# Optimization experiments

Measured on AMD Instinct MI355X. Metric: run time of the kernel, lower is better.

The kernel has to match this reference:

```python
import jax, jax.numpy as jnp
import numpy as np

D_MODEL = 4096
NUM_EXPERTS = 64
TOP_K = 2


def setup_inputs() -> dict:
    key = jax.random.key(0)
    kx, kw, kb = jax.random.split(key, 3)
    x = jax.random.normal(kx, (4, 4096, D_MODEL), dtype=jnp.float32)
    # nn.Linear(d_model, num_experts): weight [E, D], bias [E]
    bound = 1.0 / np.sqrt(D_MODEL)
    W = jax.random.uniform(kw, (NUM_EXPERTS, D_MODEL), dtype=jnp.float32, minval=-bound, maxval=bound)
    b = jax.random.uniform(kb, (NUM_EXPERTS,), dtype=jnp.float32, minval=-bound, maxval=bound)
    return {"x": x, "W": W, "b": b}


def reference(x, W, b):
    # logits = gate(x): [B, S, E]
    logits = jnp.einsum("bsd,ed->bse", x, W) + b
    scores = jax.nn.softmax(logits, axis=-1)
    topk_scores, topk_idx = jax.lax.top_k(scores, TOP_K)  # [B,S,K]
    # scatter top-k scores back into a dense [B,S,E] dispatch mask
    onehot = jax.nn.one_hot(topk_idx, NUM_EXPERTS, dtype=scores.dtype)  # [B,S,K,E]
    dispatch_mask = jnp.einsum("bske,bsk->bse", onehot, topk_scores)
    return dispatch_mask
```

## Files before the change

kernel.cpp:

```cpp
#include <hip/hip_runtime.h>
#include <hip/hip_bf16.h>
#include <math.h>
#include <stdint.h>

#define DM 4096
#define NEXP 64
#define BK 32
#define NCH (DM / BK)
#define TOKW 64
#define NSLICE 8
#define CHPS (NCH / NSLICE)
#define NTOK 16384

typedef short bf16x8 __attribute__((ext_vector_type(8)));
typedef float f32x4  __attribute__((ext_vector_type(4)));

__device__ __forceinline__ void split2(float f0, float f1, uint32_t& hw, uint32_t& lw) {
    float2 ff; ff.x = f0; ff.y = f1;
    __hip_bfloat162 h = __float22bfloat162_rn(ff);
    union { __hip_bfloat162 b; uint32_t u; } ch; ch.b = h;
    hw = ch.u;
    float h0 = __bfloat162float(h.x);
    float h1 = __bfloat162float(h.y);
    float2 gg; gg.x = f0 - h0; gg.y = f1 - h1;
    __hip_bfloat162 l = __float22bfloat162_rn(gg);
    union { __hip_bfloat162 b; uint32_t u; } cl; cl.b = l;
    lw = cl.u;
}

__global__ __launch_bounds__(256) void wsplit_kernel(const float* __restrict__ W,
                                                     char* __restrict__ blob) {
    const int c   = blockIdx.x;
    const int tid = threadIdx.x;
    const int e   = tid >> 2;
    const int g   = tid & 3;

    const float* src = W + (size_t)e * DM + c * BK + g * 8;
    float x[8];
    *(float4*)(x)     = *(const float4*)(src);
    *(float4*)(x + 4) = *(const float4*)(src + 4);

    uint32_t hiw[4], low[4];
#pragma unroll
    for (int j = 0; j < 4; ++j) split2(x[2 * j], x[2 * j + 1], hiw[j], low[j]);

    const int ln = (e & 15) | (g << 4);
    const int n4 = e >> 4;
    const size_t base = (size_t)c * 8192 + (size_t)n4 * 1024 + (size_t)ln * 16;
    *(uint4*)(blob + base)        = *(uint4*)hiw;
    *(uint4*)(blob + base + 4096) = *(uint4*)low;
}

__global__ __launch_bounds__(1024) void router_mfma_kernel(
    const float* __restrict__ X,
    const char* __restrict__ blob,
    const float* __restrict__ Bv,
    float* __restrict__ out)
{
    __shared__ float part[NSLICE][TOKW][NEXP];

    const int tid  = threadIdx.x;
    const int lane = tid & 63;
    const int wv   = tid >> 6;
    const int eh   = wv & 1;
    const int ksl  = wv >> 1;
    const long tok0 = (long)blockIdx.x * TOKW;

    const int tk = lane & 15;
    const int kg = lane >> 4;

    const float* a0 = X + (size_t)(tok0 + tk) * DM + kg * 8;

    f32x4 acc[4][2];
#pragma unroll
    for (int m = 0; m < 4; ++m)
#pragma unroll
        for (int n = 0; n < 2; ++n) acc[m][n] = (f32x4)0.0f;

    const int c0 = ksl * CHPS;
#pragma unroll 1
    for (int ci = 0; ci < CHPS; ++ci) {
        const int c = c0 + ci;

        float ar[4][8];
#pragma unroll
        for (int m = 0; m < 4; ++m) {
            const float* p = a0 + (size_t)m * (16 * DM) + c * BK;
            *(float4*)(ar[m])     = *(const float4*)(p);
            *(float4*)(ar[m] + 4) = *(const float4*)(p + 4);
        }

        bf16x8 ah[4], al[4];
#pragma unroll
        for (int m = 0; m < 4; ++m) {
            uint32_t hw[4], lw[4];
#pragma unroll
            for (int j = 0; j < 4; ++j)
                split2(ar[m][2 * j], ar[m][2 * j + 1], hw[j], lw[j]);
            ah[m] = *(bf16x8*)hw;
            al[m] = *(bf16x8*)lw;
        }

        const char* bb = blob + (size_t)c * 8192;
#pragma unroll
        for (int n = 0; n < 2; ++n) {
            const size_t bo = (size_t)(eh * 2 + n) * 1024 + (size_t)lane * 16;
            bf16x8 bh = *(const bf16x8*)(bb + bo);
            bf16x8 bl = *(const bf16x8*)(bb + 4096 + bo);
#pragma unroll
            for (int m = 0; m < 4; ++m) {
                acc[m][n] = __builtin_amdgcn_mfma_f32_16x16x32_bf16(ah[m], bh, acc[m][n], 0, 0, 0);
                acc[m][n] = __builtin_amdgcn_mfma_f32_16x16x32_bf16(ah[m], bl, acc[m][n], 0, 0, 0);
                acc[m][n] = __builtin_amdgcn_mfma_f32_16x16x32_bf16(al[m], bh, acc[m][n], 0, 0, 0);
            }
        }
    }

#pragma unroll
    for (int m = 0; m < 4; ++m)
#pragma unroll
        for (int n = 0; n < 2; ++n)
#pragma unroll
            for (int r = 0; r < 4; ++r)
                part[ksl][m * 16 + kg * 4 + r][eh * 32 + n * 16 + tk] = acc[m][n][r];
    __syncthreads();

#pragma unroll
    for (int i = 0; i < 4; ++i) {
        const int cell = tid + i * 1024;
        const int t = cell >> 6;
        const int e = cell & 63;
        float s = part[0][t][e];
#pragma unroll
        for (int w = 1; w < NSLICE; ++w) s += part[w][t][e];
        part[0][t][e] = s;
    }
    __syncthreads();

    const float bias = Bv[lane];
#pragma unroll 1
    for (int j = 0; j < 4; ++j) {
        const int t = wv * 4 + j;
        float v = part[0][t][lane] + bias;

        float m1 = v;        int i1 = lane;
        float m2 = -3.4e38f; int i2 = 127;
#pragma unroll
        for (int s = 1; s < 64; s <<= 1) {
            float om1 = __shfl_xor(m1, s, 64);
            int   oi1 = __shfl_xor(i1, s, 64);
            float om2 = __shfl_xor(m2, s, 64);
            int   oi2 = __shfl_xor(i2, s, 64);
            bool bw2 = (om1 > m1) || (om1 == m1 && oi1 < i1);
            float l1v = bw2 ? m1 : om1;  int l1i = bw2 ? i1 : oi1;
            float w2v = bw2 ? om2 : m2;  int w2i = bw2 ? oi2 : i2;
            if (bw2) { m1 = om1; i1 = oi1; }
            bool tw = (l1v > w2v) || (l1v == w2v && l1i < w2i);
            m2 = tw ? l1v : w2v;  i2 = tw ? l1i : w2i;
        }

        float p = expf(v - m1);
        float ssum = p;
#pragma unroll
        for (int s = 1; s < 64; s <<= 1) ssum += __shfl_xor(ssum, s, 64);

        float sc = (lane == i1 || lane == i2) ? (p / ssum) : 0.0f;
        out[(size_t)(tok0 + t) * NEXP + lane] = sc;
    }
}

extern "C" void kernel_launch(void* const* d_in, const int* in_sizes, int n_in,
                              void* d_out, int out_size, void* d_ws, size_t ws_size,
                              hipStream_t stream) {
    const float* X  = (const float*)d_in[0];
    const float* W  = (const float*)d_in[1];
    const float* Bv = (const float*)d_in[2];
    float* out = (float*)d_out;

    char* blob = (char*)d_ws;
    wsplit_kernel<<<dim3(NCH), dim3(256), 0, stream>>>(W, blob);

    router_mfma_kernel<<<dim3(NTOK / TOKW), dim3(1024), 0, stream>>>(X, blob, Bv, out);
}
```

Before: 85.05 us.

## Stream X tiles into LDS with async double-buffered loads and retile waves

Activation tiles are now staged into LDS using global_load_lds with a two-deep ring buffer and explicit vmcnt waits. This overlaps the global load of the next K-chunks with the fp32-to-bf16 split and the MFMA work. The block shrinks to 32 tokens and 8 waves, each wave covering all 64 experts over one K-slice, which doubles the grid and targets 4 blocks per CU. The cost is hand-tuned waitcnt counts that depend on the compiler's instruction order, more re-reads of the weight blob across blocks, and 64KB of LDS per block, which may limit occupancy.

```diff
diff --git a/kernel.cpp b/kernel.cpp
--- a/kernel.cpp
+++ b/kernel.cpp
@@ -7,13 +7,16 @@
 #define NEXP 64
 #define BK 32
 #define NCH (DM / BK)
-#define TOKW 64
-#define NSLICE 8
-#define CHPS (NCH / NSLICE)
+#define TOKW 32
+#define KSPLIT 8
+#define CHPS (NCH / KSPLIT)
 #define NTOK 16384
 
 typedef short bf16x8 __attribute__((ext_vector_type(8)));
 typedef float f32x4  __attribute__((ext_vector_type(4)));
+
+#define WAITVM12() { asm volatile("s_waitcnt vmcnt(12)" ::: "memory"); __builtin_amdgcn_sched_barrier(0); }
+#define WAITVM8()  { asm volatile("s_waitcnt vmcnt(8)"  ::: "memory"); __builtin_amdgcn_sched_barrier(0); }
 
 __device__ __forceinline__ void split2(float f0, float f1, uint32_t& hw, uint32_t& lw) {
     float2 ff; ff.x = f0; ff.y = f1;
@@ -51,97 +54,118 @@
     *(uint4*)(blob + base + 4096) = *(uint4*)low;
 }
 
-__global__ __launch_bounds__(1024) void router_mfma_kernel(
+__global__ __launch_bounds__(512, 4) void router_mfma_kernel(
     const float* __restrict__ X,
     const char* __restrict__ blob,
     const float* __restrict__ Bv,
     float* __restrict__ out)
 {
-    __shared__ float part[NSLICE][TOKW][NEXP];
+    __shared__ __align__(16) char smem[65536];
 
     const int tid  = threadIdx.x;
     const int lane = tid & 63;
     const int wv   = tid >> 6;
-    const int eh   = wv & 1;
-    const int ksl  = wv >> 1;
     const long tok0 = (long)blockIdx.x * TOKW;
 
     const int tk = lane & 15;
     const int kg = lane >> 4;
 
-    const float* a0 = X + (size_t)(tok0 + tk) * DM + kg * 8;
-
-    f32x4 acc[4][2];
-#pragma unroll
-    for (int m = 0; m < 4; ++m)
-#pragma unroll
-        for (int n = 0; n < 2; ++n) acc[m][n] = (f32x4)0.0f;
-
-    const int c0 = ksl * CHPS;
+    char* wbase = smem + wv * 8192;
+    const int c0 = wv * CHPS;
+
+    auto stage = [&](int c, int b) {
+#pragma unroll
+        for (int m = 0; m < 2; ++m)
+#pragma unroll
+            for (int h = 0; h < 2; ++h) {
+                const float* src = X + (size_t)(tok0 + m * 16 + tk) * DM + c * BK + kg * 8 + h * 4;
+                char* dst = wbase + b * 4096 + (m * 2 + h) * 1024 + lane * 16;
+                __builtin_amdgcn_global_load_lds(
+                    (const __attribute__((address_space(1))) void*)src,
+                    (__attribute__((address_space(3))) void*)dst, 16, 0, 0);
+            }
+    };
+
+    f32x4 acc[2][4];
+#pragma unroll
+    for (int m = 0; m < 2; ++m)
+#pragma unroll
+        for (int n = 0; n < 4; ++n) acc[m][n] = (f32x4)0.0f;
+
+    stage(c0 + 0, 0);
+    stage(c0 + 1, 1);
+
 #pragma unroll 1
     for (int ci = 0; ci < CHPS; ++ci) {
         const int c = c0 + ci;
-
-        float ar[4][8];
-#pragma unroll
-        for (int m = 0; m < 4; ++m) {
-            const float* p = a0 + (size_t)m * (16 * DM) + c * BK;
-            *(float4*)(ar[m])     = *(const float4*)(p);
-            *(float4*)(ar[m] + 4) = *(const float4*)(p + 4);
+        const int b = ci & 1;
+
+        const char* bb = blob + (size_t)c * 8192;
+        bf16x8 bh[4], bl[4];
+#pragma unroll
+        for (int n = 0; n < 4; ++n) {
+            const size_t bo = (size_t)n * 1024 + (size_t)lane * 16;
+            bh[n] = *(const bf16x8*)(bb + bo);
+            bl[n] = *(const bf16x8*)(bb + 4096 + bo);
         }
 
-        bf16x8 ah[4], al[4];
-#pragma unroll
-        for (int m = 0; m < 4; ++m) {
+        if (ci < CHPS - 1) { WAITVM12(); } else { WAITVM8(); }
+
+        bf16x8 ah[2], al[2];
+#pragma unroll
+        for (int m = 0; m < 2; ++m) {
+            const char* fb = wbase + b * 4096 + m * 2048 + lane * 16;
+            f32x4 f0 = *(const f32x4*)(fb);
+            f32x4 f1 = *(const f32x4*)(fb + 1024);
             uint32_t hw[4], lw[4];
-#pragma unroll
-            for (int j = 0; j < 4; ++j)
-                split2(ar[m][2 * j], ar[m][2 * j + 1], hw[j], lw[j]);
+            split2(f0.x, f0.y, hw[0], lw[0]);
+            split2(f0.z, f0.w, hw[1], lw[1]);
+            split2(f1.x, f1.y, hw[2], lw[2]);
+            split2(f1.z, f1.w, hw[3], lw[3]);
             ah[m] = *(bf16x8*)hw;
             al[m] = *(bf16x8*)lw;
         }
 
-        const char* bb = blob + (size_t)c * 8192;
-#pragma unroll
-        for (int n = 0; n < 2; ++n) {
-            const size_t bo = (size_t)(eh * 2 + n) * 1024 + (size_t)lane * 16;
-            bf16x8 bh = *(const bf16x8*)(bb + bo);
-            bf16x8 bl = *(const bf16x8*)(bb + 4096 + bo);
-#pragma unroll
-            for (int m = 0; m < 4; ++m) {
-                acc[m][n] = __builtin_amdgcn_mfma_f32_16x16x32_bf16(ah[m], bh, acc[m][n], 0, 0, 0);
-                acc[m][n] = __builtin_amdgcn_mfma_f32_16x16x32_bf16(ah[m], bl, acc[m][n], 0, 0, 0);
-                acc[m][n] = __builtin_amdgcn_mfma_f32_16x16x32_bf16(al[m], bh, acc[m][n], 0, 0, 0);
+        if (ci + 2 < CHPS) stage(c0 + ci + 2, b);
+        __builtin_amdgcn_sched_barrier(0);
+
+#pragma unroll
+        for (int n = 0; n < 4; ++n)
+#pragma unroll
+            for (int m = 0; m < 2; ++m) {
+                acc[m][n] = __builtin_amdgcn_mfma_f32_16x16x32_bf16(ah[m], bh[n], acc[m][n], 0, 0, 0);
+                acc[m][n] = __builtin_amdgcn_mfma_f32_16x16x32_bf16(ah[m], bl[n], acc[m][n], 0, 0, 0);
+                acc[m][n] = __builtin_amdgcn_mfma_f32_16x16x32_bf16(al[m], bh[n], acc[m][n], 0, 0, 0);
             }
-        }
     }
 
-#pragma unroll
-    for (int m = 0; m < 4; ++m)
-#pragma unroll
-        for (int n = 0; n < 2; ++n)
+    float* pf = (float*)smem;
+#pragma unroll
+    for (int m = 0; m < 2; ++m)
+#pragma unroll
+        for (int n = 0; n < 4; ++n)
 #pragma unroll
             for (int r = 0; r < 4; ++r)
-                part[ksl][m * 16 + kg * 4 + r][eh * 32 + n * 16 + tk] = acc[m][n][r];
+                pf[wv * 2048 + (m * 16 + kg * 4 + r) * 64 + n * 16 + tk] = acc[m][n][r];
     __syncthreads();
 
 #pragma unroll
     for (int i = 0; i < 4; ++i) {
-        const int cell = tid + i * 1024;
+        const int cell = tid + i * 512;
         const int t = cell >> 6;
         const int e = cell & 63;
-        float s = part[0][t][e];
-#pragma unroll
-        for (int w = 1; w < NSLICE; ++w) s += part[w][t][e];
-        part[0][t][e] = s;
+        float s = pf[t * 64 + e];
+#pragma unroll
+        for (int w = 1; w < KSPLIT; ++w) s += pf[w * 2048 + t * 64 + e];
+        pf[t * 64 + e] = s;
     }
     __syncthreads();
 
     const float bias = Bv[lane];
 #pragma unroll 1
-    for (int j = 0; j < 4; ++j) {
-        const int t = wv * 4 + j;
-        float v = part[0][t][lane] + bias;
+    for (int j = 0; j < TOKW / KSPLIT; ++j) {
+        const int t = wv * (TOKW / KSPLIT) + j;
+        float v = pf[t * 64 + lane] + bias;
 
         float m1 = v;        int i1 = lane;
         float m2 = -3.4e38f; int i2 = 127;
@@ -180,5 +204,5 @@
     char* blob = (char*)d_ws;
     wsplit_kernel<<<dim3(NCH), dim3(256), 0, stream>>>(W, blob);
 
-    router_mfma_kernel<<<dim3(NTOK / TOKW), dim3(1024), 0, stream>>>(X, blob, Bv, out);
-}
+    router_mfma_kernel<<<dim3(NTOK / TOKW), dim3(512), 0, stream>>>(X, blob, Bv, out);
+}
```

After: 75.09 us. 1.13x faster.

## Stage X tiles into LDS with async double-buffered loads, drop split-K reduction

Applied to the files above, without the earlier changes.

Restructures the router GEMM so each 512-thread block handles 32 tokens. X tiles are streamed into a swizzled, double-buffered LDS area with global_load_lds, and each wave owns a 16x16 output tile over the full K dimension. This removes the 8-way split-K partial-sum buffer and its reduction pass, and overlaps the global loads with MFMA work. The cost is manual vmcnt waits and barriers every step, and twice as many blocks, each of which re-reads the full weight blob.

```diff
diff --git a/kernel.cpp b/kernel.cpp
--- a/kernel.cpp
+++ b/kernel.cpp
@@ -5,11 +5,8 @@
 
 #define DM 4096
 #define NEXP 64
-#define BK 32
-#define NCH (DM / BK)
-#define TOKW 64
-#define NSLICE 8
-#define CHPS (NCH / NSLICE)
+#define TOKW 32
+#define NSTEP 32
 #define NTOK 16384
 
 typedef short bf16x8 __attribute__((ext_vector_type(8)));
@@ -35,7 +32,7 @@
     const int e   = tid >> 2;
     const int g   = tid & 3;
 
-    const float* src = W + (size_t)e * DM + c * BK + g * 8;
+    const float* src = W + (size_t)e * DM + c * 32 + g * 8;
     float x[8];
     *(float4*)(x)     = *(const float4*)(src);
     *(float4*)(x + 4) = *(const float4*)(src + 4);
@@ -51,106 +48,102 @@
     *(uint4*)(blob + base + 4096) = *(uint4*)low;
 }
 
-__global__ __launch_bounds__(1024) void router_mfma_kernel(
+__global__ __launch_bounds__(512, 4) void router_mfma_kernel(
     const float* __restrict__ X,
     const char* __restrict__ blob,
     const float* __restrict__ Bv,
     float* __restrict__ out)
 {
-    __shared__ float part[NSLICE][TOKW][NEXP];
+    __shared__ __align__(16) char smem[32768];
 
     const int tid  = threadIdx.x;
     const int lane = tid & 63;
     const int wv   = tid >> 6;
-    const int eh   = wv & 1;
-    const int ksl  = wv >> 1;
+    const int mw   = wv >> 2;
+    const int nw   = wv & 3;
     const long tok0 = (long)blockIdx.x * TOKW;
 
     const int tk = lane & 15;
     const int kg = lane >> 4;
+    const int sw = tk & 7;
 
-    const float* a0 = X + (size_t)(tok0 + tk) * DM + kg * 8;
+    auto stage = [&](int s, int b) {
+#pragma unroll
+        for (int j = 0; j < 2; ++j) {
+            const int r  = wv * 4 + j * 2 + (lane >> 5);
+            const int us = (lane & 31) ^ (r & 7);
+            const float* src = X + (size_t)(tok0 + r) * DM + s * 128 + us * 4;
+            char* dst = smem + b * 16384 + (wv * 4 + j * 2) * 512 + lane * 16;
+            __builtin_amdgcn_global_load_lds(
+                (const __attribute__((address_space(1))) void*)src,
+                (__attribute__((address_space(3))) void*)dst, 16, 0, 0);
+        }
+    };
 
-    f32x4 acc[4][2];
+    f32x4 acc = (f32x4)0.0f;
+
+    stage(0, 0);
+
+#pragma unroll 1
+    for (int s = 0; s < NSTEP; ++s) {
+        const int b = s & 1;
+
+        bf16x8 bh[4], bl[4];
+        const char* bb0 = blob + (size_t)(4 * s) * 8192 + (size_t)nw * 1024 + (size_t)lane * 16;
 #pragma unroll
-    for (int m = 0; m < 4; ++m)
-#pragma unroll
-        for (int n = 0; n < 2; ++n) acc[m][n] = (f32x4)0.0f;
-
-    const int c0 = ksl * CHPS;
-#pragma unroll 1
-    for (int ci = 0; ci < CHPS; ++ci) {
-        const int c = c0 + ci;
-
-        float ar[4][8];
-#pragma unroll
-        for (int m = 0; m < 4; ++m) {
-            const float* p = a0 + (size_t)m * (16 * DM) + c * BK;
-            *(float4*)(ar[m])     = *(const float4*)(p);
-            *(float4*)(ar[m] + 4) = *(const float4*)(p + 4);
+        for (int ks = 0; ks < 4; ++ks) {
+            bh[ks] = *(const bf16x8*)(bb0 + ks * 8192);
+            bl[ks] = *(const bf16x8*)(bb0 + ks * 8192 + 4096);
         }
 
-        bf16x8 ah[4], al[4];
+        if (s + 1 < NSTEP) stage(s + 1, b ^ 1);
+
+        if (s + 1 < NSTEP) { asm volatile("s_waitcnt vmcnt(10)" ::: "memory"); }
+        else               { asm volatile("s_waitcnt vmcnt(8)"  ::: "memory"); }
+        __builtin_amdgcn_sched_barrier(0);
+        __builtin_amdgcn_s_barrier();
+
+        const char* rb = smem + b * 16384 + (mw * 16 + tk) * 512;
 #pragma unroll
-        for (int m = 0; m < 4; ++m) {
+        for (int ks = 0; ks < 4; ++ks) {
+            const int v = ks * 8 + kg * 2;
+            f32x4 r0 = *(const f32x4*)(rb + ((v       ^ sw) * 16));
+            f32x4 r1 = *(const f32x4*)(rb + (((v + 1) ^ sw) * 16));
             uint32_t hw[4], lw[4];
-#pragma unroll
-            for (int j = 0; j < 4; ++j)
-                split2(ar[m][2 * j], ar[m][2 * j + 1], hw[j], lw[j]);
-            ah[m] = *(bf16x8*)hw;
-            al[m] = *(bf16x8*)lw;
+            split2(r0.x, r0.y, hw[0], lw[0]);
+            split2(r0.z, r0.w, hw[1], lw[1]);
+            split2(r1.x, r1.y, hw[2], lw[2]);
+            split2(r1.z, r1.w, hw[3], lw[3]);
+            bf16x8 ah = *(bf16x8*)hw;
+            bf16x8 al = *(bf16x8*)lw;
+            acc = __builtin_amdgcn_mfma_f32_16x16x32_bf16(ah, bh[ks], acc, 0, 0, 0);
+            acc = __builtin_amdgcn_mfma_f32_16x16x32_bf16(ah, bl[ks], acc, 0, 0, 0);
+            acc = __builtin_amdgcn_mfma_f32_16x16x32_bf16(al, bh[ks], acc, 0, 0, 0);
         }
 
-        const char* bb = blob + (size_t)c * 8192;
-#pragma unroll
-        for (int n = 0; n < 2; ++n) {
-            const size_t bo = (size_t)(eh * 2 + n) * 1024 + (size_t)lane * 16;
-            bf16x8 bh = *(const bf16x8*)(bb + bo);
-            bf16x8 bl = *(const bf16x8*)(bb + 4096 + bo);
-#pragma unroll
-            for (int m = 0; m < 4; ++m) {
-                acc[m][n] = __builtin_amdgcn_mfma_f32_16x16x32_bf16(ah[m], bh, acc[m][n], 0, 0, 0);
-                acc[m][n] = __builtin_amdgcn_mfma_f32_16x16x32_bf16(ah[m], bl, acc[m][n], 0, 0, 0);
-                acc[m][n] = __builtin_amdgcn_mfma_f32_16x16x32_bf16(al[m], bh, acc[m][n], 0, 0, 0);
-            }
-        }
+        __builtin_amdgcn_s_barrier();
     }
 
+    float* pf = (float*)smem;
 #pragma unroll
-    for (int m = 0; m < 4; ++m)
-#pragma unroll
-        for (int n = 0; n < 2; ++n)
-#pragma unroll
-            for (int r = 0; r < 4; ++r)
-                part[ksl][m * 16 + kg * 4 + r][eh * 32 + n * 16 + tk] = acc[m][n][r];
-    __syncthreads();
-
-#pragma unroll
-    for (int i = 0; i < 4; ++i) {
-        const int cell = tid + i * 1024;
-        const int t = cell >> 6;
-        const int e = cell & 63;
-        float s = part[0][t][e];
-#pragma unroll
-        for (int w = 1; w < NSLICE; ++w) s += part[w][t][e];
-        part[0][t][e] = s;
-    }
+    for (int r = 0; r < 4; ++r)
+        pf[(mw * 16 + kg * 4 + r) * 64 + nw * 16 + tk] = acc[r];
     __syncthreads();
 
     const float bias = Bv[lane];
 #pragma unroll 1
     for (int j = 0; j < 4; ++j) {
         const int t = wv * 4 + j;
-        float v = part[0][t][lane] + bias;
+        float v = pf[t * 64 + lane] + bias;
 
         float m1 = v;        int i1 = lane;
         float m2 = -3.4e38f; int i2 = 127;
 #pragma unroll
-        for (int s = 1; s < 64; s <<= 1) {
-            float om1 = __shfl_xor(m1, s, 64);
-            int   oi1 = __shfl_xor(i1, s, 64);
-            float om2 = __shfl_xor(m2, s, 64);
-            int   oi2 = __shfl_xor(i2, s, 64);
+        for (int s2 = 1; s2 < 64; s2 <<= 1) {
+            float om1 = __shfl_xor(m1, s2, 64);
+            int   oi1 = __shfl_xor(i1, s2, 64);
+            float om2 = __shfl_xor(m2, s2, 64);
+            int   oi2 = __shfl_xor(i2, s2, 64);
             bool bw2 = (om1 > m1) || (om1 == m1 && oi1 < i1);
             float l1v = bw2 ? m1 : om1;  int l1i = bw2 ? i1 : oi1;
             float w2v = bw2 ? om2 : m2;  int w2i = bw2 ? oi2 : i2;
@@ -162,7 +155,7 @@
         float p = expf(v - m1);
         float ssum = p;
 #pragma unroll
-        for (int s = 1; s < 64; s <<= 1) ssum += __shfl_xor(ssum, s, 64);
+        for (int s2 = 1; s2 < 64; s2 <<= 1) ssum += __shfl_xor(ssum, s2, 64);
 
         float sc = (lane == i1 || lane == i2) ? (p / ssum) : 0.0f;
         out[(size_t)(tok0 + t) * NEXP + lane] = sc;
@@ -178,7 +171,7 @@
     float* out = (float*)d_out;
 
     char* blob = (char*)d_ws;
-    wsplit_kernel<<<dim3(NCH), dim3(256), 0, stream>>>(W, blob);
+    wsplit_kernel<<<dim3(128), dim3(256), 0, stream>>>(W, blob);
 
-    router_mfma_kernel<<<dim3(NTOK / TOKW), dim3(1024), 0, stream>>>(X, blob, Bv, out);
+    router_mfma_kernel<<<dim3(NTOK / TOKW), dim3(512), 0, stream>>>(X, blob, Bv, out);
 }
```

Measured after the change: 97.00 us. 14.1% more time.
